# Kernel optimization log

Measured on AMD Instinct MI355X. Metric: run time of the kernel, lower is better.

Reference implementation:

```python
import jax, jax.numpy as jnp
import numpy as np

N_NODES = 100000
N_EDGES = 3200000
IN_F, HID, OUT_F = 128, 3, 4


def setup_inputs() -> dict:
    key = jax.random.key(0)
    k1, k2, k3, k4, k5, k6 = jax.random.split(key, 6)
    x = jax.random.normal(k1, (N_NODES, IN_F), dtype=jnp.float32)
    edge_index = jax.random.randint(k2, (2, N_EDGES), 0, N_NODES, dtype=jnp.int64)
    # GCNConv weight (glorot) + bias, Linear(3,4) weight + bias
    W = jax.random.normal(k3, (IN_F, HID), dtype=jnp.float32) * (1.0 / np.sqrt(IN_F))
    b = jnp.zeros((HID,), dtype=jnp.float32)
    Wout = jax.random.normal(k4, (HID, OUT_F), dtype=jnp.float32) * (1.0 / np.sqrt(HID))
    bout = jax.random.normal(k5, (OUT_F,), dtype=jnp.float32) * 0.01
    return {"x": x, "edge_index": edge_index, "W": W, "b": b, "Wout": Wout, "bout": bout}


def reference(x, edge_index, W, b, Wout, bout):
    N = x.shape[0]
    # add self loops (PyG GCNConv default: add_self_loops=True)
    loop = jnp.arange(N, dtype=edge_index.dtype)
    row = jnp.concatenate([edge_index[0], loop])  # source nodes
    col = jnp.concatenate([edge_index[1], loop])  # destination nodes
    # linear transform first (cheaper: 128 -> 3)
    xw = x @ W  # [N, 3]
    # symmetric degree normalization: deg computed on destination index
    deg = jax.ops.segment_sum(jnp.ones_like(col, dtype=x.dtype), col, num_segments=N)
    dinv = jnp.where(deg > 0, jax.lax.rsqrt(deg), 0.0)
    norm = dinv[row] * dinv[col]  # [E+N]
    # gather source features, scale, scatter-add to destinations
    msg = xw[row] * norm[:, None]  # [E+N, 3]
    agg = jax.ops.segment_sum(msg, col, num_segments=N)  # [N, 3]
    h = jax.nn.relu(agg + b)
    z = h @ Wout + bout
    return (h, z)
```

## Files before the change

kernel.cpp:

```cpp
#include <hip/hip_runtime.h>

#define N_NODES 100000
#define N_EDGES 3200000
#define IN_F    128
#define HID     3
#define OUT_F   4

#define BSHIFT  7
#define BSIZE   128
#define NBUCK   ((N_NODES + BSIZE - 1) / BSIZE)
#define NBLKA   512
#define EPB     ((N_EDGES + NBLKA - 1) / NBLKA)
#define NH      (NBUCK * NBLKA)

#define SCAN_ITEMS 16
#define SCAN_BLOCK 256
#define SCAN_PER_BLOCK (SCAN_ITEMS * SCAN_BLOCK)
#define NS1 ((NH + SCAN_PER_BLOCK - 1) / SCAN_PER_BLOCK)


__global__ void xw_kernel(const float* __restrict__ x,
                          const float* __restrict__ W,
                          float* __restrict__ xw) {
    int wave = threadIdx.x >> 6;
    int lane = threadIdx.x & 63;
    int half = lane >> 5;
    int l    = lane & 31;
    int node = blockIdx.x * 8 + wave * 2 + half;
    if (node >= N_NODES) return;

    float4 xv = *reinterpret_cast<const float4*>(x + (size_t)node * IN_F + l * 4);
    const float* w = W + l * 4 * HID;
    float s0 = xv.x * w[0] + xv.y * w[3] + xv.z * w[6] + xv.w * w[9];
    float s1 = xv.x * w[1] + xv.y * w[4] + xv.z * w[7] + xv.w * w[10];
    float s2 = xv.x * w[2] + xv.y * w[5] + xv.z * w[8] + xv.w * w[11];
    #pragma unroll
    for (int off = 16; off > 0; off >>= 1) {
        s0 += __shfl_down(s0, off, 32);
        s1 += __shfl_down(s1, off, 32);
        s2 += __shfl_down(s2, off, 32);
    }
    if (l == 0) {
        xw[node * 3 + 0] = s0;
        xw[node * 3 + 1] = s1;
        xw[node * 3 + 2] = s2;
    }
}

__global__ void histA_kernel(const int* __restrict__ col, int* __restrict__ histG) {
    __shared__ int hist[NBUCK];
    int tid = threadIdx.x, blk = blockIdx.x;
    for (int i = tid; i < NBUCK; i += 256) hist[i] = 0;
    __syncthreads();
    int start = blk * EPB, end = min(start + EPB, N_EDGES);
    for (int e = start + tid; e < end; e += 256)
        atomicAdd(&hist[col[e] >> BSHIFT], 1);
    __syncthreads();
    for (int i = tid; i < NBUCK; i += 256)
        histG[i * NBLKA + blk] = hist[i];
}

__global__ void scan1_kernel(int* __restrict__ data, int* __restrict__ bsum) {
    __shared__ int s[SCAN_BLOCK];
    int tid = threadIdx.x;
    int base = blockIdx.x * SCAN_PER_BLOCK + tid * SCAN_ITEMS;
    int v[SCAN_ITEMS];
    int tsum = 0;
    #pragma unroll
    for (int j = 0; j < SCAN_ITEMS; ++j) {
        v[j] = (base + j < NH) ? data[base + j] : 0;
        tsum += v[j];
    }
    s[tid] = tsum;
    __syncthreads();
    for (int off = 1; off < SCAN_BLOCK; off <<= 1) {
        int t = (tid >= off) ? s[tid - off] : 0;
        __syncthreads();
        s[tid] += t;
        __syncthreads();
    }
    int run = s[tid] - tsum;
    #pragma unroll
    for (int j = 0; j < SCAN_ITEMS; ++j) {
        int t = v[j];
        if (base + j < NH) data[base + j] = run;
        run += t;
    }
    if (tid == SCAN_BLOCK - 1) bsum[blockIdx.x] = s[SCAN_BLOCK - 1];
}

__global__ void scan2_kernel(int* __restrict__ bsum) {
    __shared__ int s[SCAN_BLOCK];
    int tid = threadIdx.x;
    int v = (tid < NS1) ? bsum[tid] : 0;
    s[tid] = v;
    __syncthreads();
    for (int off = 1; off < SCAN_BLOCK; off <<= 1) {
        int t = (tid >= off) ? s[tid - off] : 0;
        __syncthreads();
        s[tid] += t;
        __syncthreads();
    }
    if (tid < NS1) bsum[tid] = s[tid] - v;
}

__global__ void scan3_kernel(int* __restrict__ data, const int* __restrict__ bsum) {
    int i = blockIdx.x * blockDim.x + threadIdx.x;
    if (i < NH) data[i] += bsum[i / SCAN_PER_BLOCK];
}

__global__ void fillB_kernel(const int* __restrict__ row,
                             const int* __restrict__ col,
                             const int* __restrict__ histG,
                             int* __restrict__ packed) {
    __shared__ int offs[NBUCK];
    int tid = threadIdx.x, blk = blockIdx.x;
    for (int i = tid; i < NBUCK; i += 256) offs[i] = histG[i * NBLKA + blk];
    __syncthreads();
    int start = blk * EPB, end = min(start + EPB, N_EDGES);
    for (int e = start + tid; e < end; e += 256) {
        int c = col[e], r = row[e];
        int b = c >> BSHIFT;
        int pos = atomicAdd(&offs[b], 1);
        packed[pos] = (r << BSHIFT) | (c & (BSIZE - 1));
    }
}

__global__ __launch_bounds__(512) void degC_kernel(const int* __restrict__ histG,
                                                   const int* __restrict__ packed,
                                                   const float* __restrict__ xw,
                                                   float4* __restrict__ xwn4) {
    __shared__ int cnt[BSIZE];
    int tid = threadIdx.x, b = blockIdx.x;
    if (tid < BSIZE) cnt[tid] = 0;
    __syncthreads();
    int start = histG[b * NBLKA];
    int end   = (b + 1 < NBUCK) ? histG[(b + 1) * NBLKA] : N_EDGES;
    int len   = end - start;
    int nfull = len & ~(4 * 512 - 1);
    for (int off = tid; off < nfull; off += 2048) {
        int p0 = packed[start + off];
        int p1 = packed[start + off + 512];
        int p2 = packed[start + off + 1024];
        int p3 = packed[start + off + 1536];
        atomicAdd(&cnt[p0 & (BSIZE - 1)], 1);
        atomicAdd(&cnt[p1 & (BSIZE - 1)], 1);
        atomicAdd(&cnt[p2 & (BSIZE - 1)], 1);
        atomicAdd(&cnt[p3 & (BSIZE - 1)], 1);
    }
    for (int off = nfull + tid; off < len; off += 512)
        atomicAdd(&cnt[packed[start + off] & (BSIZE - 1)], 1);
    __syncthreads();
    if (tid < BSIZE) {
        int node = b * BSIZE + tid;
        if (node < N_NODES) {
            float d = rsqrtf((float)(cnt[tid] + 1));
            xwn4[node] = make_float4(xw[node * 3 + 0] * d,
                                     xw[node * 3 + 1] * d,
                                     xw[node * 3 + 2] * d, d);
        }
    }
}

__global__ __launch_bounds__(512) void aggC_kernel(const int* __restrict__ histG,
                                                   const int* __restrict__ packed,
                                                   const float4* __restrict__ xwn4,
                                                   const float* __restrict__ bb,
                                                   const float* __restrict__ Wout,
                                                   const float* __restrict__ bout,
                                                   float* __restrict__ out) {
    __shared__ float acc[BSIZE * 3];
    int tid = threadIdx.x, b = blockIdx.x;
    for (int i = tid; i < BSIZE * 3; i += 512) acc[i] = 0.f;
    __syncthreads();
    int start = histG[b * NBLKA];
    int end   = (b + 1 < NBUCK) ? histG[(b + 1) * NBLKA] : N_EDGES;
    int len   = end - start;
    int nfull = len & ~(4 * 512 - 1);
    for (int off = tid; off < nfull; off += 2048) {
        int p0 = packed[start + off];
        int p1 = packed[start + off + 512];
        int p2 = packed[start + off + 1024];
        int p3 = packed[start + off + 1536];
        float4 v0 = xwn4[p0 >> BSHIFT];
        float4 v1 = xwn4[p1 >> BSHIFT];
        float4 v2 = xwn4[p2 >> BSHIFT];
        float4 v3 = xwn4[p3 >> BSHIFT];
        int c0 = (p0 & (BSIZE - 1)) * 3, c1 = (p1 & (BSIZE - 1)) * 3;
        int c2 = (p2 & (BSIZE - 1)) * 3, c3 = (p3 & (BSIZE - 1)) * 3;
        atomicAdd(&acc[c0 + 0], v0.x); atomicAdd(&acc[c0 + 1], v0.y); atomicAdd(&acc[c0 + 2], v0.z);
        atomicAdd(&acc[c1 + 0], v1.x); atomicAdd(&acc[c1 + 1], v1.y); atomicAdd(&acc[c1 + 2], v1.z);
        atomicAdd(&acc[c2 + 0], v2.x); atomicAdd(&acc[c2 + 1], v2.y); atomicAdd(&acc[c2 + 2], v2.z);
        atomicAdd(&acc[c3 + 0], v3.x); atomicAdd(&acc[c3 + 1], v3.y); atomicAdd(&acc[c3 + 2], v3.z);
    }
    for (int off = nfull + tid; off < len; off += 512) {
        int p = packed[start + off];
        float4 v = xwn4[p >> BSHIFT];
        int c = (p & (BSIZE - 1)) * 3;
        atomicAdd(&acc[c + 0], v.x);
        atomicAdd(&acc[c + 1], v.y);
        atomicAdd(&acc[c + 2], v.z);
    }
    __syncthreads();
    if (tid < BSIZE) {
        int node = b * BSIZE + tid;
        if (node < N_NODES) {
            float4 s = xwn4[node];
            float di = s.w;
            float h0 = fmaxf((acc[tid * 3 + 0] + s.x) * di + bb[0], 0.f);
            float h1 = fmaxf((acc[tid * 3 + 1] + s.y) * di + bb[1], 0.f);
            float h2 = fmaxf((acc[tid * 3 + 2] + s.z) * di + bb[2], 0.f);
            out[node * 3 + 0] = h0;
            out[node * 3 + 1] = h1;
            out[node * 3 + 2] = h2;
            float* z = out + (size_t)N_NODES * 3;
            #pragma unroll
            for (int k = 0; k < 4; ++k) {
                z[node * 4 + k] = bout[k] + h0 * Wout[0 * 4 + k]
                                          + h1 * Wout[1 * 4 + k]
                                          + h2 * Wout[2 * 4 + k];
            }
        }
    }
}

extern "C" void kernel_launch(void* const* d_in, const int* in_sizes, int n_in,
                              void* d_out, int out_size, void* d_ws, size_t ws_size,
                              hipStream_t stream) {
    const float* x    = (const float*)d_in[0];
    const int*   ei   = (const int*)d_in[1];
    const float* W    = (const float*)d_in[2];
    const float* b    = (const float*)d_in[3];
    const float* Wout = (const float*)d_in[4];
    const float* bout = (const float*)d_in[5];
    float* out = (float*)d_out;

    char* wsb = (char*)d_ws;
    int*    histG  = (int*)(wsb);
    int*    packed = (int*)(wsb + (size_t)NH * 4);
    float*  xw     = (float*)(wsb + (size_t)NH * 4 + (size_t)N_EDGES * 4);
    float4* xwn4   = (float4*)((char*)xw + (size_t)N_NODES * 3 * 4);
    int*    bsum   = (int*)((char*)xwn4 + (size_t)N_NODES * 16);

    const int* row = ei;
    const int* col = ei + N_EDGES;

    const int B = 256;
    int gridX  = (N_NODES + 7) / 8;
    int gridS3 = (NH + B - 1) / B;

    xw_kernel<<<gridX, B, 0, stream>>>(x, W, xw);
    histA_kernel<<<NBLKA, B, 0, stream>>>(col, histG);
    scan1_kernel<<<NS1, SCAN_BLOCK, 0, stream>>>(histG, bsum);
    scan2_kernel<<<1, SCAN_BLOCK, 0, stream>>>(bsum);
    scan3_kernel<<<gridS3, B, 0, stream>>>(histG, bsum);
    fillB_kernel<<<NBLKA, B, 0, stream>>>(row, col, histG, packed);
    degC_kernel<<<NBUCK, 512, 0, stream>>>(histG, packed, xw, xwn4);
    aggC_kernel<<<NBUCK, 512, 0, stream>>>(histG, packed, xwn4, b, Wout, bout, out);
}
```

Baseline: 233.1 us.

## Use fp16 gather table, replicated LDS accumulators, and nontemporal streaming loads

The per-node normalized feature table is stored as four fp16 values (8 bytes) instead of a float4, which halves the bytes touched by the random gather in the aggregation kernel. Shared-memory histogram and accumulator arrays are replicated four ways, with padded strides, to reduce LDS atomic contention, and the copies are summed at the end. Streaming reads and writes of x, the edge lists and the packed array use nontemporal hints so they do not pollute the cache, and launch bounds request higher occupancy. The fp16 storage loses precision in the messages and could exceed the output tolerance.

```diff
diff --git a/kernel.cpp b/kernel.cpp
--- a/kernel.cpp
+++ b/kernel.cpp
@@ -1,4 +1,5 @@
 #include <hip/hip_runtime.h>
+#include <hip/hip_fp16.h>
 
 #define N_NODES 100000
 #define N_EDGES 3200000
@@ -17,6 +18,12 @@
 #define SCAN_BLOCK 256
 #define SCAN_PER_BLOCK (SCAN_ITEMS * SCAN_BLOCK)
 #define NS1 ((NH + SCAN_PER_BLOCK - 1) / SCAN_PER_BLOCK)
+
+#define NREP    4
+#define RSTRIDE 392
+#define CSTRIDE 136
+
+typedef float f32x4 __attribute__((ext_vector_type(4)));
 
 
 __global__ void xw_kernel(const float* __restrict__ x,
@@ -29,7 +36,8 @@
     int node = blockIdx.x * 8 + wave * 2 + half;
     if (node >= N_NODES) return;
 
-    float4 xv = *reinterpret_cast<const float4*>(x + (size_t)node * IN_F + l * 4);
+    f32x4 xv = __builtin_nontemporal_load(
+        reinterpret_cast<const f32x4*>(x + (size_t)node * IN_F + l * 4));
     const float* w = W + l * 4 * HID;
     float s0 = xv.x * w[0] + xv.y * w[3] + xv.z * w[6] + xv.w * w[9];
     float s1 = xv.x * w[1] + xv.y * w[4] + xv.z * w[7] + xv.w * w[10];
@@ -54,7 +62,7 @@
     __syncthreads();
     int start = blk * EPB, end = min(start + EPB, N_EDGES);
     for (int e = start + tid; e < end; e += 256)
-        atomicAdd(&hist[col[e] >> BSHIFT], 1);
+        atomicAdd(&hist[__builtin_nontemporal_load(&col[e]) >> BSHIFT], 1);
     __syncthreads();
     for (int i = tid; i < NBUCK; i += 256)
         histG[i * NBLKA + blk] = hist[i];
@@ -119,97 +127,128 @@
     __syncthreads();
     int start = blk * EPB, end = min(start + EPB, N_EDGES);
     for (int e = start + tid; e < end; e += 256) {
-        int c = col[e], r = row[e];
+        int c = __builtin_nontemporal_load(&col[e]);
+        int r = __builtin_nontemporal_load(&row[e]);
         int b = c >> BSHIFT;
         int pos = atomicAdd(&offs[b], 1);
-        packed[pos] = (r << BSHIFT) | (c & (BSIZE - 1));
-    }
-}
-
-__global__ __launch_bounds__(512) void degC_kernel(const int* __restrict__ histG,
-                                                   const int* __restrict__ packed,
-                                                   const float* __restrict__ xw,
-                                                   float4* __restrict__ xwn4) {
-    __shared__ int cnt[BSIZE];
+        __builtin_nontemporal_store((r << BSHIFT) | (c & (BSIZE - 1)), &packed[pos]);
+    }
+}
+
+__global__ __launch_bounds__(512, 8) void degC_kernel(const int* __restrict__ histG,
+                                                      const int* __restrict__ packed,
+                                                      const float* __restrict__ xw,
+                                                      uint2* __restrict__ tab) {
+    __shared__ int cnt[NREP * CSTRIDE];
     int tid = threadIdx.x, b = blockIdx.x;
-    if (tid < BSIZE) cnt[tid] = 0;
+    int rep = tid & (NREP - 1);
+    for (int i = tid; i < NREP * CSTRIDE; i += 512) cnt[i] = 0;
     __syncthreads();
     int start = histG[b * NBLKA];
     int end   = (b + 1 < NBUCK) ? histG[(b + 1) * NBLKA] : N_EDGES;
     int len   = end - start;
     int nfull = len & ~(4 * 512 - 1);
     for (int off = tid; off < nfull; off += 2048) {
-        int p0 = packed[start + off];
-        int p1 = packed[start + off + 512];
-        int p2 = packed[start + off + 1024];
-        int p3 = packed[start + off + 1536];
-        atomicAdd(&cnt[p0 & (BSIZE - 1)], 1);
-        atomicAdd(&cnt[p1 & (BSIZE - 1)], 1);
-        atomicAdd(&cnt[p2 & (BSIZE - 1)], 1);
-        atomicAdd(&cnt[p3 & (BSIZE - 1)], 1);
+        int p0 = __builtin_nontemporal_load(&packed[start + off]);
+        int p1 = __builtin_nontemporal_load(&packed[start + off + 512]);
+        int p2 = __builtin_nontemporal_load(&packed[start + off + 1024]);
+        int p3 = __builtin_nontemporal_load(&packed[start + off + 1536]);
+        atomicAdd(&cnt[rep * CSTRIDE + (p0 & (BSIZE - 1))], 1);
+        atomicAdd(&cnt[rep * CSTRIDE + (p1 & (BSIZE - 1))], 1);
+        atomicAdd(&cnt[rep * CSTRIDE + (p2 & (BSIZE - 1))], 1);
+        atomicAdd(&cnt[rep * CSTRIDE + (p3 & (BSIZE - 1))], 1);
     }
     for (int off = nfull + tid; off < len; off += 512)
-        atomicAdd(&cnt[packed[start + off] & (BSIZE - 1)], 1);
+        atomicAdd(&cnt[rep * CSTRIDE + (__builtin_nontemporal_load(&packed[start + off]) & (BSIZE - 1))], 1);
     __syncthreads();
     if (tid < BSIZE) {
         int node = b * BSIZE + tid;
         if (node < N_NODES) {
-            float d = rsqrtf((float)(cnt[tid] + 1));
-            xwn4[node] = make_float4(xw[node * 3 + 0] * d,
-                                     xw[node * 3 + 1] * d,
-                                     xw[node * 3 + 2] * d, d);
+            int c = cnt[0 * CSTRIDE + tid] + cnt[1 * CSTRIDE + tid]
+                  + cnt[2 * CSTRIDE + tid] + cnt[3 * CSTRIDE + tid];
+            float d = rsqrtf((float)(c + 1));
+            __half2 lo = __floats2half2_rn(xw[node * 3 + 0] * d, xw[node * 3 + 1] * d);
+            __half2 hi = __floats2half2_rn(xw[node * 3 + 2] * d, d);
+            uint2 u;
+            u.x = *reinterpret_cast<unsigned int*>(&lo);
+            u.y = *reinterpret_cast<unsigned int*>(&hi);
+            tab[node] = u;
         }
     }
 }
 
-__global__ __launch_bounds__(512) void aggC_kernel(const int* __restrict__ histG,
-                                                   const int* __restrict__ packed,
-                                                   const float4* __restrict__ xwn4,
-                                                   const float* __restrict__ bb,
-                                                   const float* __restrict__ Wout,
-                                                   const float* __restrict__ bout,
-                                                   float* __restrict__ out) {
-    __shared__ float acc[BSIZE * 3];
+__device__ inline void unpack4(uint2 u, float& a, float& b, float& c, float& d) {
+    __half2 lo = *reinterpret_cast<__half2*>(&u.x);
+    __half2 hi = *reinterpret_cast<__half2*>(&u.y);
+    float2 f0 = __half22float2(lo);
+    float2 f1 = __half22float2(hi);
+    a = f0.x; b = f0.y; c = f1.x; d = f1.y;
+}
+
+__global__ __launch_bounds__(512, 8) void aggC_kernel(const int* __restrict__ histG,
+                                                      const int* __restrict__ packed,
+                                                      const uint2* __restrict__ tab,
+                                                      const float* __restrict__ bb,
+                                                      const float* __restrict__ Wout,
+                                                      const float* __restrict__ bout,
+                                                      float* __restrict__ out) {
+    __shared__ float acc[NREP * RSTRIDE];
     int tid = threadIdx.x, b = blockIdx.x;
-    for (int i = tid; i < BSIZE * 3; i += 512) acc[i] = 0.f;
+    int rep = tid & (NREP - 1);
+    float* myacc = acc + rep * RSTRIDE;
+    for (int i = tid; i < NREP * RSTRIDE; i += 512) acc[i] = 0.f;
     __syncthreads();
     int start = histG[b * NBLKA];
     int end   = (b + 1 < NBUCK) ? histG[(b + 1) * NBLKA] : N_EDGES;
     int len   = end - start;
     int nfull = len & ~(4 * 512 - 1);
     for (int off = tid; off < nfull; off += 2048) {
-        int p0 = packed[start + off];
-        int p1 = packed[start + off + 512];
-        int p2 = packed[start + off + 1024];
-        int p3 = packed[start + off + 1536];
-        float4 v0 = xwn4[p0 >> BSHIFT];
-        float4 v1 = xwn4[p1 >> BSHIFT];
-        float4 v2 = xwn4[p2 >> BSHIFT];
-        float4 v3 = xwn4[p3 >> BSHIFT];
-        int c0 = (p0 & (BSIZE - 1)) * 3, c1 = (p1 & (BSIZE - 1)) * 3;
-        int c2 = (p2 & (BSIZE - 1)) * 3, c3 = (p3 & (BSIZE - 1)) * 3;
-        atomicAdd(&acc[c0 + 0], v0.x); atomicAdd(&acc[c0 + 1], v0.y); atomicAdd(&acc[c0 + 2], v0.z);
-        atomicAdd(&acc[c1 + 0], v1.x); atomicAdd(&acc[c1 + 1], v1.y); atomicAdd(&acc[c1 + 2], v1.z);
-        atomicAdd(&acc[c2 + 0], v2.x); atomicAdd(&acc[c2 + 1], v2.y); atomicAdd(&acc[c2 + 2], v2.z);
-        atomicAdd(&acc[c3 + 0], v3.x); atomicAdd(&acc[c3 + 1], v3.y); atomicAdd(&acc[c3 + 2], v3.z);
+        int p0 = __builtin_nontemporal_load(&packed[start + off]);
+        int p1 = __builtin_nontemporal_load(&packed[start + off + 512]);
+        int p2 = __builtin_nontemporal_load(&packed[start + off + 1024]);
+        int p3 = __builtin_nontemporal_load(&packed[start + off + 1536]);
+        uint2 u0 = tab[p0 >> BSHIFT];
+        uint2 u1 = tab[p1 >> BSHIFT];
+        uint2 u2 = tab[p2 >> BSHIFT];
+        uint2 u3 = tab[p3 >> BSHIFT];
+        float a0, b0, c0, d0, a1, b1, c1, d1, a2, b2, c2, d2, a3, b3, c3, d3;
+        unpack4(u0, a0, b0, c0, d0);
+        unpack4(u1, a1, b1, c1, d1);
+        unpack4(u2, a2, b2, c2, d2);
+        unpack4(u3, a3, b3, c3, d3);
+        int i0 = (p0 & (BSIZE - 1)) * 3, i1 = (p1 & (BSIZE - 1)) * 3;
+        int i2 = (p2 & (BSIZE - 1)) * 3, i3 = (p3 & (BSIZE - 1)) * 3;
+        atomicAdd(&myacc[i0 + 0], a0); atomicAdd(&myacc[i0 + 1], b0); atomicAdd(&myacc[i0 + 2], c0);
+        atomicAdd(&myacc[i1 + 0], a1); atomicAdd(&myacc[i1 + 1], b1); atomicAdd(&myacc[i1 + 2], c1);
+        atomicAdd(&myacc[i2 + 0], a2); atomicAdd(&myacc[i2 + 1], b2); atomicAdd(&myacc[i2 + 2], c2);
+        atomicAdd(&myacc[i3 + 0], a3); atomicAdd(&myacc[i3 + 1], b3); atomicAdd(&myacc[i3 + 2], c3);
     }
     for (int off = nfull + tid; off < len; off += 512) {
-        int p = packed[start + off];
-        float4 v = xwn4[p >> BSHIFT];
-        int c = (p & (BSIZE - 1)) * 3;
-        atomicAdd(&acc[c + 0], v.x);
-        atomicAdd(&acc[c + 1], v.y);
-        atomicAdd(&acc[c + 2], v.z);
+        int p = __builtin_nontemporal_load(&packed[start + off]);
+        uint2 u = tab[p >> BSHIFT];
+        float a, bq, c, d;
+        unpack4(u, a, bq, c, d);
+        int i = (p & (BSIZE - 1)) * 3;
+        atomicAdd(&myacc[i + 0], a);
+        atomicAdd(&myacc[i + 1], bq);
+        atomicAdd(&myacc[i + 2], c);
     }
     __syncthreads();
     if (tid < BSIZE) {
         int node = b * BSIZE + tid;
         if (node < N_NODES) {
-            float4 s = xwn4[node];
-            float di = s.w;
-            float h0 = fmaxf((acc[tid * 3 + 0] + s.x) * di + bb[0], 0.f);
-            float h1 = fmaxf((acc[tid * 3 + 1] + s.y) * di + bb[1], 0.f);
-            float h2 = fmaxf((acc[tid * 3 + 2] + s.z) * di + bb[2], 0.f);
+            float sx, sy, sz, di;
+            unpack4(tab[node], sx, sy, sz, di);
+            float g0 = sx, g1 = sy, g2 = sz;
+            #pragma unroll
+            for (int rr = 0; rr < NREP; ++rr) {
+                g0 += acc[rr * RSTRIDE + tid * 3 + 0];
+                g1 += acc[rr * RSTRIDE + tid * 3 + 1];
+                g2 += acc[rr * RSTRIDE + tid * 3 + 2];
+            }
+            float h0 = fmaxf(g0 * di + bb[0], 0.f);
+            float h1 = fmaxf(g1 * di + bb[1], 0.f);
+            float h2 = fmaxf(g2 * di + bb[2], 0.f);
             out[node * 3 + 0] = h0;
             out[node * 3 + 1] = h1;
             out[node * 3 + 2] = h2;
@@ -236,11 +275,11 @@
     float* out = (float*)d_out;
 
     char* wsb = (char*)d_ws;
-    int*    histG  = (int*)(wsb);
-    int*    packed = (int*)(wsb + (size_t)NH * 4);
-    float*  xw     = (float*)(wsb + (size_t)NH * 4 + (size_t)N_EDGES * 4);
-    float4* xwn4   = (float4*)((char*)xw + (size_t)N_NODES * 3 * 4);
-    int*    bsum   = (int*)((char*)xwn4 + (size_t)N_NODES * 16);
+    int*   histG  = (int*)(wsb);
+    int*   packed = (int*)(wsb + (size_t)NH * 4);
+    float* xw     = (float*)(wsb + (size_t)NH * 4 + (size_t)N_EDGES * 4);
+    uint2* tab    = (uint2*)((char*)xw + (size_t)N_NODES * 3 * 4);
+    int*   bsum   = (int*)((char*)tab + (size_t)N_NODES * 8);
 
     const int* row = ei;
     const int* col = ei + N_EDGES;
@@ -255,6 +294,6 @@
     scan2_kernel<<<1, SCAN_BLOCK, 0, stream>>>(bsum);
     scan3_kernel<<<gridS3, B, 0, stream>>>(histG, bsum);
     fillB_kernel<<<NBLKA, B, 0, stream>>>(row, col, histG, packed);
-    degC_kernel<<<NBUCK, 512, 0, stream>>>(histG, packed, xw, xwn4);
-    aggC_kernel<<<NBUCK, 512, 0, stream>>>(histG, packed, xwn4, b, Wout, bout, out);
-}
+    degC_kernel<<<NBUCK, 512, 0, stream>>>(histG, packed, xw, tab);
+    aggC_kernel<<<NBUCK, 512, 0, stream>>>(histG, packed, tab, b, Wout, bout, out);
+}
```

New measurement: 302.5 us. 29.8% more time.
